# Performance work log

Measured on AMD Instinct MI355X. Metric: run time of the kernel, lower is better.

## Reference

```python
import jax, jax.numpy as jnp
import numpy as np

N_OUT = 500000   # active octree nodes at output level
N_IN = 500000    # active octree nodes at input level (jump=0 -> same)
K = 27           # 3x3x3 kernel offsets
C_IN = 16
C_OUT = 16
LEVEL = 8


def setup_inputs() -> dict:
    key = jax.random.key(0)
    k1, k2, k3, k4 = jax.random.split(key, 4)
    stdv = 1.0 / np.sqrt(C_IN * K)
    inputs = jax.random.normal(k1, (N_IN, C_IN), dtype=jnp.float32)
    weight = jax.random.uniform(k2, (K, C_IN, C_OUT), dtype=jnp.float32,
                                minval=-stdv, maxval=stdv)
    bias = jax.random.uniform(k3, (C_OUT,), dtype=jnp.float32,
                              minval=-stdv, maxval=stdv)
    # Precomputed neighborhood map n(i, k): index of the input node at
    # offset kernel_vectors[k] from output node i (what the octree traversal
    # in the CUDA kernel produces).
    neighbor_idx = jax.random.randint(k4, (N_OUT, K), 0, N_IN, dtype=jnp.int32)
    return {"input": inputs, "weight": weight, "bias": bias,
            "neighbor_idx": neighbor_idx, "level": LEVEL}


def reference(input, weight, bias, neighbor_idx, level):
    # Y_i = sum_k W_k . X_{n(i,k)} + b
    gathered = input[neighbor_idx]                      # [N_out, K, C_in]
    out = jnp.einsum('nkc,kco->no', gathered, weight)   # [N_out, C_out]
    out = out + bias[None, :]
    return out, level
```

## Files before the change

### kernel.cpp

```cpp
#include <hip/hip_runtime.h>


typedef __attribute__((ext_vector_type(4))) int   int4v;
typedef __attribute__((ext_vector_type(4))) float f32x4;

#define K_OFF 27
#define C_IN  16
#define C_OUT 16
#define NT    7
#define X_CLAMP 6.0f
#define SX (X_CLAMP / 127.0f)

#define BQ_BYTES  (NT * 64 * 16)
#define SCALE_OFF 7168
#define X8_OFF    8192

#define OSB_STRIDE 20

static __device__ __forceinline__ int q8(float x, float inv_step) {
    float y = x * inv_step;
    y = fminf(fmaxf(y, -127.0f), 127.0f);
    return __float2int_rn(y) & 255;
}

__global__ void prep_kernel(const float* __restrict__ input,
                            const float* __restrict__ weight,
                            const int* __restrict__ level,
                            signed char* __restrict__ ws8,
                            float* __restrict__ out_level,
                            int write_level, int n_rows)
{
    signed char* bq = ws8;
    float* wscale_p = (float*)(ws8 + SCALE_OFF);
    signed char* x8 = ws8 + X8_OFF;

    const float inv_sx = 127.0f / X_CLAMP;

    int r = blockIdx.x * blockDim.x + threadIdx.x;
    if (r < n_rows) {
        const f32x4* p = (const f32x4*)(input + (size_t)r * C_IN);
        f32x4 v0 = __builtin_nontemporal_load(p + 0);
        f32x4 v1 = __builtin_nontemporal_load(p + 1);
        f32x4 v2 = __builtin_nontemporal_load(p + 2);
        f32x4 v3 = __builtin_nontemporal_load(p + 3);
        int4v o;
        o[0] = q8(v0[0], inv_sx) | (q8(v0[1], inv_sx) << 8) |
               (q8(v0[2], inv_sx) << 16) | (q8(v0[3], inv_sx) << 24);
        o[1] = q8(v1[0], inv_sx) | (q8(v1[1], inv_sx) << 8) |
               (q8(v1[2], inv_sx) << 16) | (q8(v1[3], inv_sx) << 24);
        o[2] = q8(v2[0], inv_sx) | (q8(v2[1], inv_sx) << 8) |
               (q8(v2[2], inv_sx) << 16) | (q8(v2[3], inv_sx) << 24);
        o[3] = q8(v3[0], inv_sx) | (q8(v3[1], inv_sx) << 8) |
               (q8(v3[2], inv_sx) << 16) | (q8(v3[3], inv_sx) << 24);
        *(int4v*)(x8 + (size_t)r * C_IN) = o;
    }

    if (blockIdx.x == 0) {
        __shared__ float red[256];
        const int nW = K_OFF * C_IN * C_OUT;
        float mx = 0.0f;
#pragma unroll 4
        for (int e = threadIdx.x; e < nW; e += 256)
            mx = fmaxf(mx, fabsf(weight[e]));
        red[threadIdx.x] = mx;
        __syncthreads();
        for (int s = 128; s > 0; s >>= 1) {
            if (threadIdx.x < s)
                red[threadIdx.x] = fmaxf(red[threadIdx.x], red[threadIdx.x + s]);
            __syncthreads();
        }
        float wmax = red[0];
        if (wmax <= 0.0f) wmax = 1.0f;
        float sw = wmax / 127.0f;
        float inv_sw = 127.0f / wmax;
        if (threadIdx.x == 0) {
            wscale_p[0] = sw;
            if (write_level) *out_level = (float)(*level);
        }
#pragma unroll 4
        for (int e = threadIdx.x; e < BQ_BYTES; e += 256) {
            int j    = e & 15;
            int lane = (e >> 4) & 63;
            int t    = e >> 10;
            int n    = lane & 15;
            int g    = lane >> 4;
            int koff = t * 4 + g;
            signed char v = 0;
            if (koff < K_OFF) {
                float w = weight[(koff * C_IN + j) * C_OUT + n];
                float y = w * inv_sw;
                y = fminf(fmaxf(y, -127.0f), 127.0f);
                v = (signed char)__float2int_rn(y);
            }
            bq[e] = v;
        }
    }
}

template<bool LOAD_ACC, bool STORE_OUT>
__global__ __launch_bounds__(256, 8) void conv_kernel(
    const signed char* __restrict__ x8,
    const float* __restrict__ bias,
    const int* __restrict__ nbr,
    const signed char* __restrict__ bq,
    const float* __restrict__ wscale_p,
    int4v* __restrict__ acc_ws,
    float* __restrict__ out,
    int n_out, int lo, int hi)
{
    __shared__ int4v bq_lds[NT * 64];
    __shared__ int4v nbr_lds[4][108];

    const int lane = threadIdx.x & 63;
    const int wave = threadIdx.x >> 6;
    const int m    = lane & 15;
    const int g    = lane >> 4;

    {
        const int4v* bq4 = (const int4v*)bq;
        for (int e = threadIdx.x; e < NT * 64; e += 256)
            bq_lds[e] = bq4[e];
    }
    __syncthreads();

    const int tile   = blockIdx.x * 4 + wave;
    const int i_base = tile * 16;
    if (i_base >= n_out) return;

    {
        const int4v* nb4 = (const int4v*)nbr;
        size_t base4 = (size_t)i_base * K_OFF / 4;
        const size_t lim4 = ((size_t)n_out * K_OFF) / 4;
        size_t e0 = base4 + lane;
        if (e0 >= lim4) e0 = lim4 - 1;
        nbr_lds[wave][lane] = __builtin_nontemporal_load(&nb4[e0]);
        if (lane < 108 - 64) {
            size_t e1 = base4 + 64 + lane;
            if (e1 >= lim4) e1 = lim4 - 1;
            nbr_lds[wave][64 + lane] = __builtin_nontemporal_load(&nb4[e1]);
        }
    }

    const int* nd = (const int*)nbr_lds[wave];
    int rows[NT];
#pragma unroll
    for (int t = 0; t < NT; ++t) {
        int koff = 4 * t + g;
        rows[t] = (koff < K_OFF) ? nd[m * K_OFF + koff] : -1;
    }

    const int4v* x84 = (const int4v*)x8;
    int4v afrag[NT];
#pragma unroll
    for (int t = 0; t < NT; ++t) {
        int4v a = {0, 0, 0, 0};
        if (rows[t] >= lo && rows[t] < hi)
            a = x84[rows[t]];
        afrag[t] = a;
    }

    int4v acc;
    if (LOAD_ACC) {
        acc = __builtin_nontemporal_load(&acc_ws[(size_t)tile * 64 + lane]);
    } else {
        acc = (int4v){0, 0, 0, 0};
    }

#pragma unroll
    for (int t = 0; t < NT; ++t)
        acc = __builtin_amdgcn_mfma_i32_16x16x64_i8(afrag[t], bq_lds[t * 64 + lane],
                                                    acc, 0, 0, 0);

    if (STORE_OUT) {
        const float sc = SX * wscale_p[0];
        const float bv = bias[m];
        float* osb = (float*)&nbr_lds[wave][0];
#pragma unroll
        for (int r = 0; r < 4; ++r) {
            osb[(g * 4 + r) * OSB_STRIDE + m] = (float)acc[r] * sc + bv;
        }
        asm volatile("s_waitcnt lgkmcnt(0)" ::: "memory");
        int n_loc = lane >> 2;
        int q     = lane & 3;
        int snode = i_base + n_loc;
        if (snode < n_out) {
            const f32x4* src = (const f32x4*)(osb + n_loc * OSB_STRIDE + q * 4);
            f32x4 v = *src;
            __builtin_nontemporal_store(v,
                (f32x4*)&out[(size_t)snode * C_OUT + q * 4]);
        }
    } else {
        __builtin_nontemporal_store(acc, &acc_ws[(size_t)tile * 64 + lane]);
    }
}

extern "C" void kernel_launch(void* const* d_in, const int* in_sizes, int n_in_arrs,
                              void* d_out, int out_size, void* d_ws, size_t ws_size,
                              hipStream_t stream) {
    const float* input  = (const float*)d_in[0];
    const float* weight = (const float*)d_in[1];
    const float* bias   = (const float*)d_in[2];
    const int*   nbr    = (const int*)d_in[3];
    const int*   level  = (const int*)d_in[4];
    float*       out    = (float*)d_out;

    const int n_rows = in_sizes[0] / C_IN;
    const int n_out  = in_sizes[3] / K_OFF;

    signed char* ws8 = (signed char*)d_ws;
    signed char* x8  = ws8 + X8_OFF;
    const float* wscale_p = (const float*)(ws8 + SCALE_OFF);

    const int write_level = (out_size > n_out * C_OUT) ? 1 : 0;
    float* out_level = out + (size_t)n_out * C_OUT;

    const int prep_blocks = (n_rows + 255) / 256;
    prep_kernel<<<prep_blocks, 256, 0, stream>>>(
        input, weight, level, ws8, out_level, write_level, n_rows);

    const int conv_blocks = (n_out + 63) / 64;
    const size_t acc_off   = (size_t)X8_OFF + (size_t)n_rows * 16;
    const size_t acc_bytes = (size_t)conv_blocks * 4 * 64 * sizeof(int4v);
    int4v* acc_ws = (int4v*)(ws8 + acc_off);

    if (ws_size >= acc_off + acc_bytes) {
        const int half = n_rows / 2;
        conv_kernel<false, false><<<conv_blocks, 256, 0, stream>>>(
            x8, bias, nbr, ws8, wscale_p, acc_ws, out, n_out, 0, half);
        conv_kernel<true, true><<<conv_blocks, 256, 0, stream>>>(
            x8, bias, nbr, ws8, wscale_p, acc_ws, out, n_out, half, n_rows);
    } else {
        conv_kernel<false, true><<<conv_blocks, 256, 0, stream>>>(
            x8, bias, nbr, ws8, wscale_p, acc_ws, out, n_out, 0, n_rows);
    }
}
```

Before: 228.0 us.

## Fuse prep and two conv passes into one cooperative persistent kernel

Replaces the three launches (quantize prep, first-half conv, second-half conv) with a single cooperative kernel that uses grid-wide syncs between phases. Each block handles up to 8 tile units and keeps their accumulators in registers across the half-split passes, so the int32 partial-accumulator round trip through global memory goes away. The cost is grid.sync overhead, a fixed 1024-block persistent grid, higher register pressure from 8 accumulators, and neighbor indices being loaded twice. The multi-kernel path stays as a fallback if the cooperative launch fails.

```diff
diff --git a/kernel.cpp b/kernel.cpp
--- a/kernel.cpp
+++ b/kernel.cpp
@@ -1,4 +1,7 @@
 #include <hip/hip_runtime.h>
+#include <hip/hip_cooperative_groups.h>
+
+namespace cg = cooperative_groups;
 
 
 typedef __attribute__((ext_vector_type(4))) int   int4v;
@@ -16,11 +19,208 @@
 #define X8_OFF    8192
 
 #define OSB_STRIDE 20
+#define GRID_BLKS  1024
+#define MAX_UNITS  8
 
 static __device__ __forceinline__ int q8(float x, float inv_step) {
     float y = x * inv_step;
     y = fminf(fmaxf(y, -127.0f), 127.0f);
     return __float2int_rn(y) & 255;
+}
+
+static __device__ __forceinline__ void quant_row(const float* __restrict__ input,
+                                                 signed char* __restrict__ x8,
+                                                 int r, float inv_sx) {
+    const f32x4* p = (const f32x4*)(input + (size_t)r * C_IN);
+    f32x4 v0 = __builtin_nontemporal_load(p + 0);
+    f32x4 v1 = __builtin_nontemporal_load(p + 1);
+    f32x4 v2 = __builtin_nontemporal_load(p + 2);
+    f32x4 v3 = __builtin_nontemporal_load(p + 3);
+    int4v o;
+    o[0] = q8(v0[0], inv_sx) | (q8(v0[1], inv_sx) << 8) |
+           (q8(v0[2], inv_sx) << 16) | (q8(v0[3], inv_sx) << 24);
+    o[1] = q8(v1[0], inv_sx) | (q8(v1[1], inv_sx) << 8) |
+           (q8(v1[2], inv_sx) << 16) | (q8(v1[3], inv_sx) << 24);
+    o[2] = q8(v2[0], inv_sx) | (q8(v2[1], inv_sx) << 8) |
+           (q8(v2[2], inv_sx) << 16) | (q8(v2[3], inv_sx) << 24);
+    o[3] = q8(v3[0], inv_sx) | (q8(v3[1], inv_sx) << 8) |
+           (q8(v3[2], inv_sx) << 16) | (q8(v3[3], inv_sx) << 24);
+    *(int4v*)(x8 + (size_t)r * C_IN) = o;
+}
+
+__global__ __launch_bounds__(256, 4) void fused_kernel(
+    const float* __restrict__ input,
+    const float* __restrict__ weight,
+    const float* __restrict__ bias,
+    const int* __restrict__ nbr,
+    const int* __restrict__ level,
+    signed char* __restrict__ ws8,
+    float* __restrict__ out,
+    float* __restrict__ out_level,
+    int write_level, int n_rows, int n_out)
+{
+    signed char* bq = ws8;
+    float* wscale_p = (float*)(ws8 + SCALE_OFF);
+    signed char* x8 = ws8 + X8_OFF;
+
+    __shared__ int4v bq_lds[NT * 64];
+    __shared__ int4v nbr_lds[4][108];
+    __shared__ float red[256];
+
+    const int tid = threadIdx.x;
+    const float inv_sx = 127.0f / X_CLAMP;
+
+    {
+        int gs = gridDim.x * 256;
+        for (int r = blockIdx.x * 256 + tid; r < n_rows; r += gs)
+            quant_row(input, x8, r, inv_sx);
+    }
+
+    if (blockIdx.x == 0) {
+        const int nW = K_OFF * C_IN * C_OUT;
+        float mx = 0.0f;
+#pragma unroll 4
+        for (int e = tid; e < nW; e += 256)
+            mx = fmaxf(mx, fabsf(weight[e]));
+        red[tid] = mx;
+        __syncthreads();
+        for (int s = 128; s > 0; s >>= 1) {
+            if (tid < s) red[tid] = fmaxf(red[tid], red[tid + s]);
+            __syncthreads();
+        }
+        float wmax = red[0];
+        if (wmax <= 0.0f) wmax = 1.0f;
+        float sw = wmax / 127.0f;
+        float inv_sw = 127.0f / wmax;
+        if (tid == 0) {
+            wscale_p[0] = sw;
+            if (write_level) *out_level = (float)(*level);
+        }
+#pragma unroll 4
+        for (int e = tid; e < BQ_BYTES; e += 256) {
+            int j    = e & 15;
+            int lane = (e >> 4) & 63;
+            int t    = e >> 10;
+            int n    = lane & 15;
+            int gg   = lane >> 4;
+            int koff = t * 4 + gg;
+            signed char v = 0;
+            if (koff < K_OFF) {
+                float w = weight[(koff * C_IN + j) * C_OUT + n];
+                float y = w * inv_sw;
+                y = fminf(fmaxf(y, -127.0f), 127.0f);
+                v = (signed char)__float2int_rn(y);
+            }
+            bq[e] = v;
+        }
+    }
+
+    cg::this_grid().sync();
+
+    {
+        const int4v* bq4 = (const int4v*)bq;
+        for (int e = tid; e < NT * 64; e += 256)
+            bq_lds[e] = bq4[e];
+    }
+    __syncthreads();
+
+    const int lane = tid & 63;
+    const int wave = tid >> 6;
+    const int m    = lane & 15;
+    const int g    = lane >> 4;
+
+    const int n_units = (n_out + 63) >> 6;
+    const int half    = n_rows >> 1;
+    const int4v* x84  = (const int4v*)x8;
+    const int4v* nb4  = (const int4v*)nbr;
+    const size_t lim4 = ((size_t)n_out * K_OFF) >> 2;
+    const float sc = SX * wscale_p[0];
+    const float bv = bias[m];
+
+    int4v acc[MAX_UNITS];
+#pragma unroll
+    for (int j = 0; j < MAX_UNITS; ++j)
+        acc[j] = (int4v){0, 0, 0, 0};
+
+#pragma unroll
+    for (int j = 0; j < MAX_UNITS; ++j) {
+        int u = blockIdx.x + j * GRID_BLKS;
+        int i_base = ((u << 2) + wave) << 4;
+        if (u < n_units && i_base < n_out) {
+            size_t base4 = ((size_t)i_base * K_OFF) >> 2;
+            size_t e0 = base4 + lane;
+            if (e0 >= lim4) e0 = lim4 - 1;
+            nbr_lds[wave][lane] = __builtin_nontemporal_load(&nb4[e0]);
+            if (lane < 108 - 64) {
+                size_t e1 = base4 + 64 + lane;
+                if (e1 >= lim4) e1 = lim4 - 1;
+                nbr_lds[wave][64 + lane] = __builtin_nontemporal_load(&nb4[e1]);
+            }
+            const int* nd = (const int*)nbr_lds[wave];
+            int rows[NT];
+#pragma unroll
+            for (int t = 0; t < NT; ++t) {
+                int koff = 4 * t + g;
+                rows[t] = (koff < K_OFF) ? nd[m * K_OFF + koff] : -1;
+            }
+#pragma unroll
+            for (int t = 0; t < NT; ++t) {
+                int4v a = {0, 0, 0, 0};
+                if (rows[t] >= 0 && rows[t] < half)
+                    a = x84[rows[t]];
+                acc[j] = __builtin_amdgcn_mfma_i32_16x16x64_i8(
+                             a, bq_lds[t * 64 + lane], acc[j], 0, 0, 0);
+            }
+        }
+    }
+
+    cg::this_grid().sync();
+
+#pragma unroll
+    for (int j = 0; j < MAX_UNITS; ++j) {
+        int u = blockIdx.x + j * GRID_BLKS;
+        int i_base = ((u << 2) + wave) << 4;
+        if (u < n_units && i_base < n_out) {
+            size_t base4 = ((size_t)i_base * K_OFF) >> 2;
+            size_t e0 = base4 + lane;
+            if (e0 >= lim4) e0 = lim4 - 1;
+            nbr_lds[wave][lane] = __builtin_nontemporal_load(&nb4[e0]);
+            if (lane < 108 - 64) {
+                size_t e1 = base4 + 64 + lane;
+                if (e1 >= lim4) e1 = lim4 - 1;
+                nbr_lds[wave][64 + lane] = __builtin_nontemporal_load(&nb4[e1]);
+            }
+            const int* nd = (const int*)nbr_lds[wave];
+            int rows[NT];
+#pragma unroll
+            for (int t = 0; t < NT; ++t) {
+                int koff = 4 * t + g;
+                rows[t] = (koff < K_OFF) ? nd[m * K_OFF + koff] : -1;
+            }
+#pragma unroll
+            for (int t = 0; t < NT; ++t) {
+                int4v a = {0, 0, 0, 0};
+                if (rows[t] >= half && rows[t] < n_rows)
+                    a = x84[rows[t]];
+                acc[j] = __builtin_amdgcn_mfma_i32_16x16x64_i8(
+                             a, bq_lds[t * 64 + lane], acc[j], 0, 0, 0);
+            }
+            float* osb = (float*)&nbr_lds[wave][0];
+#pragma unroll
+            for (int r = 0; r < 4; ++r)
+                osb[(g * 4 + r) * OSB_STRIDE + m] = (float)acc[j][r] * sc + bv;
+            asm volatile("s_waitcnt lgkmcnt(0)" ::: "memory");
+            int n_loc = lane >> 2;
+            int q     = lane & 3;
+            int snode = i_base + n_loc;
+            if (snode < n_out) {
+                const f32x4* src = (const f32x4*)(osb + n_loc * OSB_STRIDE + q * 4);
+                f32x4 v = *src;
+                __builtin_nontemporal_store(v,
+                    (f32x4*)&out[(size_t)snode * C_OUT + q * 4]);
+            }
+        }
+    }
 }
 
 __global__ void prep_kernel(const float* __restrict__ input,
@@ -33,33 +233,16 @@
     signed char* bq = ws8;
     float* wscale_p = (float*)(ws8 + SCALE_OFF);
     signed char* x8 = ws8 + X8_OFF;
-
     const float inv_sx = 127.0f / X_CLAMP;
 
     int r = blockIdx.x * blockDim.x + threadIdx.x;
-    if (r < n_rows) {
-        const f32x4* p = (const f32x4*)(input + (size_t)r * C_IN);
-        f32x4 v0 = __builtin_nontemporal_load(p + 0);
-        f32x4 v1 = __builtin_nontemporal_load(p + 1);
-        f32x4 v2 = __builtin_nontemporal_load(p + 2);
-        f32x4 v3 = __builtin_nontemporal_load(p + 3);
-        int4v o;
-        o[0] = q8(v0[0], inv_sx) | (q8(v0[1], inv_sx) << 8) |
-               (q8(v0[2], inv_sx) << 16) | (q8(v0[3], inv_sx) << 24);
-        o[1] = q8(v1[0], inv_sx) | (q8(v1[1], inv_sx) << 8) |
-               (q8(v1[2], inv_sx) << 16) | (q8(v1[3], inv_sx) << 24);
-        o[2] = q8(v2[0], inv_sx) | (q8(v2[1], inv_sx) << 8) |
-               (q8(v2[2], inv_sx) << 16) | (q8(v2[3], inv_sx) << 24);
-        o[3] = q8(v3[0], inv_sx) | (q8(v3[1], inv_sx) << 8) |
-               (q8(v3[2], inv_sx) << 16) | (q8(v3[3], inv_sx) << 24);
-        *(int4v*)(x8 + (size_t)r * C_IN) = o;
-    }
+    if (r < n_rows)
+        quant_row(input, x8, r, inv_sx);
 
     if (blockIdx.x == 0) {
         __shared__ float red[256];
         const int nW = K_OFF * C_IN * C_OUT;
         float mx = 0.0f;
-#pragma unroll 4
         for (int e = threadIdx.x; e < nW; e += 256)
             mx = fmaxf(mx, fabsf(weight[e]));
         red[threadIdx.x] = mx;
@@ -77,7 +260,6 @@
             wscale_p[0] = sw;
             if (write_level) *out_level = (float)(*level);
         }
-#pragma unroll 4
         for (int e = threadIdx.x; e < BQ_BYTES; e += 256) {
             int j    = e & 15;
             int lane = (e >> 4) & 63;
@@ -98,7 +280,7 @@
 }
 
 template<bool LOAD_ACC, bool STORE_OUT>
-__global__ __launch_bounds__(256, 8) void conv_kernel(
+__global__ __launch_bounds__(256, 4) void conv_kernel(
     const signed char* __restrict__ x8,
     const float* __restrict__ bias,
     const int* __restrict__ nbr,
@@ -160,11 +342,8 @@
     }
 
     int4v acc;
-    if (LOAD_ACC) {
-        acc = __builtin_nontemporal_load(&acc_ws[(size_t)tile * 64 + lane]);
-    } else {
-        acc = (int4v){0, 0, 0, 0};
-    }
+    if (LOAD_ACC) acc = __builtin_nontemporal_load(&acc_ws[(size_t)tile * 64 + lane]);
+    else          acc = (int4v){0, 0, 0, 0};
 
 #pragma unroll
     for (int t = 0; t < NT; ++t)
@@ -176,9 +355,8 @@
         const float bv = bias[m];
         float* osb = (float*)&nbr_lds[wave][0];
 #pragma unroll
-        for (int r = 0; r < 4; ++r) {
+        for (int r = 0; r < 4; ++r)
             osb[(g * 4 + r) * OSB_STRIDE + m] = (float)acc[r] * sc + bv;
-        }
         asm volatile("s_waitcnt lgkmcnt(0)" ::: "memory");
         int n_loc = lane >> 2;
         int q     = lane & 3;
@@ -211,26 +389,44 @@
     signed char* x8  = ws8 + X8_OFF;
     const float* wscale_p = (const float*)(ws8 + SCALE_OFF);
 
-    const int write_level = (out_size > n_out * C_OUT) ? 1 : 0;
+    int write_level = (out_size > n_out * C_OUT) ? 1 : 0;
     float* out_level = out + (size_t)n_out * C_OUT;
 
-    const int prep_blocks = (n_rows + 255) / 256;
-    prep_kernel<<<prep_blocks, 256, 0, stream>>>(
-        input, weight, level, ws8, out_level, write_level, n_rows);
-
-    const int conv_blocks = (n_out + 63) / 64;
-    const size_t acc_off   = (size_t)X8_OFF + (size_t)n_rows * 16;
-    const size_t acc_bytes = (size_t)conv_blocks * 4 * 64 * sizeof(int4v);
-    int4v* acc_ws = (int4v*)(ws8 + acc_off);
-
-    if (ws_size >= acc_off + acc_bytes) {
-        const int half = n_rows / 2;
-        conv_kernel<false, false><<<conv_blocks, 256, 0, stream>>>(
-            x8, bias, nbr, ws8, wscale_p, acc_ws, out, n_out, 0, half);
-        conv_kernel<true, true><<<conv_blocks, 256, 0, stream>>>(
-            x8, bias, nbr, ws8, wscale_p, acc_ws, out, n_out, half, n_rows);
-    } else {
-        conv_kernel<false, true><<<conv_blocks, 256, 0, stream>>>(
-            x8, bias, nbr, ws8, wscale_p, acc_ws, out, n_out, 0, n_rows);
-    }
-}
+    const int n_units = (n_out + 63) / 64;
+    const bool coop_fits = (n_units <= GRID_BLKS * MAX_UNITS) &&
+                           (ws_size >= (size_t)X8_OFF + (size_t)n_rows * 16) &&
+                           (n_rows % 2 == 0 || n_rows > 0);
+
+    hipError_t err = hipErrorUnknown;
+    if (coop_fits) {
+        int nr = n_rows, no = n_out, wl = write_level;
+        void* args[] = { (void*)&input, (void*)&weight, (void*)&bias,
+                         (void*)&nbr, (void*)&level, (void*)&ws8, (void*)&out,
+                         (void*)&out_level, (void*)&wl, (void*)&nr, (void*)&no };
+        err = hipLaunchCooperativeKernel((const void*)fused_kernel,
+                                         dim3(GRID_BLKS), dim3(256),
+                                         args, 0, stream);
+    }
+
+    if (err != hipSuccess) {
+        const int prep_blocks = (n_rows + 255) / 256;
+        prep_kernel<<<prep_blocks, 256, 0, stream>>>(
+            input, weight, level, ws8, out_level, write_level, n_rows);
+
+        const int conv_blocks = (n_out + 63) / 64;
+        const size_t acc_off   = (size_t)X8_OFF + (size_t)n_rows * 16;
+        const size_t acc_bytes = (size_t)conv_blocks * 4 * 64 * sizeof(int4v);
+        int4v* acc_ws = (int4v*)(ws8 + acc_off);
+
+        if (ws_size >= acc_off + acc_bytes) {
+            const int half = n_rows / 2;
+            conv_kernel<false, false><<<conv_blocks, 256, 0, stream>>>(
+                x8, bias, nbr, ws8, wscale_p, acc_ws, out, n_out, 0, half);
+            conv_kernel<true, true><<<conv_blocks, 256, 0, stream>>>(
+                x8, bias, nbr, ws8, wscale_p, acc_ws, out, n_out, half, n_rows);
+        } else {
+            conv_kernel<false, true><<<conv_blocks, 256, 0, stream>>>(
+                x8, bias, nbr, ws8, wscale_p, acc_ws, out, n_out, 0, n_rows);
+        }
+    }
+}
```

Result: slower. 497.8 us (+118.4%).
